# Kernel optimization log

Hardware: AMD Instinct MI355X
Metric: run time of the kernel (lower is better)

The kernel has to match this reference:

```python
import jax, jax.numpy as jnp
import numpy as np

B, N_TOKENS, E = 64, 512, 512   # batch, document tokens, embedding_dim
MAX_SEQ_LEN = 64                # decode steps


def setup_inputs() -> dict:
    key = jax.random.key(0)
    ks = jax.random.split(key, 11)
    s = 0.05
    return {
        "token_embeddings": jax.random.normal(ks[0], (B, N_TOKENS, 2 * E), jnp.float32),
        "encoded_document": jax.random.normal(ks[1], (B, 2 * E), jnp.float32),
        # LSTMCell params (hidden state is zero every step, so W_hh is dead; biases still add)
        "W_ih": jax.random.normal(ks[2], (4 * E, 2 * E), jnp.float32) * s,
        "b_ih": jax.random.normal(ks[3], (4 * E,), jnp.float32) * s,
        "b_hh": jax.random.normal(ks[4], (4 * E,), jnp.float32) * s,
        # decoder_weights: Linear(E, E)
        "Wd": jax.random.normal(ks[5], (E, E), jnp.float32) * s,
        "bd": jax.random.normal(ks[6], (E,), jnp.float32) * s,
        # encoder_weights: Linear(2E, E)
        "We": jax.random.normal(ks[7], (E, 2 * E), jnp.float32) * s,
        "be": jax.random.normal(ks[8], (E,), jnp.float32) * s,
        # reference: Linear(E, 1)
        "wr": jax.random.normal(ks[9], (1, E), jnp.float32) * s,
        "br": jax.random.normal(ks[10], (1,), jnp.float32) * s,
    }


def reference(token_embeddings, encoded_document, W_ih, b_ih, b_hh, Wd, bd, We, be, wr, br):
    b = token_embeddings.shape[0]
    batch_idx = jnp.arange(b)
    # encoder projection is loop-invariant: hoist it (same math as per-step recompute)
    enc = jnp.einsum('bnd,ed->bne', token_embeddings, We) + be  # [B, N, E]

    def lstm_zero_state(x):
        # PyTorch LSTMCell with default (zero) h, c each call
        gates = x @ W_ih.T + b_ih + b_hh  # [B, 4E]
        i, f, g, o = jnp.split(gates, 4, axis=-1)
        c = jax.nn.sigmoid(i) * jnp.tanh(g)
        return jax.nn.sigmoid(o) * jnp.tanh(c)

    def step(dec_in, _):
        hx = lstm_zero_state(dec_in)              # [B, E]
        q = hx @ Wd.T + bd                        # [B, E]
        comp = jnp.tanh(q[:, None, :] + enc)      # [B, N, E]
        scores = jnp.einsum('bne,e->bn', comp, wr[0]) + br[0]  # [B, N]
        logp = jax.nn.log_softmax(scores, axis=1)
        idx = jnp.argmax(logp, axis=1)            # [B]
        nxt = token_embeddings[batch_idx, idx]    # [B, 2E]
        return nxt, (logp, idx)

    _, (probs, idxs) = jax.lax.scan(step, encoded_document, None, length=MAX_SEQ_LEN)
    overall_probabilities = jnp.transpose(probs, (1, 0, 2))  # [B, MAX_SEQ_LEN, N]
    peak_indices = idxs.T                                     # [B, MAX_SEQ_LEN]
    return overall_probabilities, peak_indices
```

## Files before the change

kernel.cpp:

```cpp
#include <hip/hip_runtime.h>


#define DEV __device__ __forceinline__

DEV float sigm(float x) { return __fdividef(1.0f, 1.0f + __expf(-x)); }
DEV float tanh_fast(float x) {
  float e = __expf(2.0f * x);
  return 1.0f - __fdividef(2.0f, e + 1.0f);
}

#define FMA4(acc, xv, wv)                                                      \
  acc = fmaf((xv).x, (wv).x, acc); acc = fmaf((xv).y, (wv).y, acc);            \
  acc = fmaf((xv).z, (wv).z, acc); acc = fmaf((xv).w, (wv).w, acc)

__global__ __launch_bounds__(256) void kenc(const float* __restrict__ A,
                                            const float* __restrict__ Bm,
                                            const float* __restrict__ bias,
                                            float* __restrict__ C) {
  __shared__ float a_s[16][132];
  __shared__ float b_s[16][132];
  const int t = threadIdx.x;
  const int row = t >> 1;
  const int kq = (t & 1) * 8;
  const float* Arow = A + (blockIdx.x * 128 + row) * 1024 + kq;
  const float* Brow = Bm + (blockIdx.y * 128 + row) * 1024 + kq;
  const int tx = t & 15, ty = t >> 4;
  float acc[8][8] = {};
  for (int k0 = 0; k0 < 1024; k0 += 16) {
    float4 av0 = *(const float4*)(Arow + k0);
    float4 av1 = *(const float4*)(Arow + k0 + 4);
    float4 bv0 = *(const float4*)(Brow + k0);
    float4 bv1 = *(const float4*)(Brow + k0 + 4);
    __syncthreads();
    a_s[kq+0][row]=av0.x; a_s[kq+1][row]=av0.y; a_s[kq+2][row]=av0.z; a_s[kq+3][row]=av0.w;
    a_s[kq+4][row]=av1.x; a_s[kq+5][row]=av1.y; a_s[kq+6][row]=av1.z; a_s[kq+7][row]=av1.w;
    b_s[kq+0][row]=bv0.x; b_s[kq+1][row]=bv0.y; b_s[kq+2][row]=bv0.z; b_s[kq+3][row]=bv0.w;
    b_s[kq+4][row]=bv1.x; b_s[kq+5][row]=bv1.y; b_s[kq+6][row]=bv1.z; b_s[kq+7][row]=bv1.w;
    __syncthreads();
    #pragma unroll
    for (int k = 0; k < 16; ++k) {
      float a[8], b[8];
      *(float4*)(a)   = *(const float4*)&a_s[k][ty*8];
      *(float4*)(a+4) = *(const float4*)&a_s[k][ty*8+4];
      *(float4*)(b)   = *(const float4*)&b_s[k][tx*8];
      *(float4*)(b+4) = *(const float4*)&b_s[k][tx*8+4];
      #pragma unroll
      for (int i = 0; i < 8; ++i)
        #pragma unroll
        for (int j = 0; j < 8; ++j)
          acc[i][j] = fmaf(a[i], b[j], acc[i][j]);
    }
  }
  const int mb = blockIdx.x * 128 + ty * 8;
  const int eb = blockIdx.y * 128 + tx * 8;
  float bv[8];
  #pragma unroll
  for (int j = 0; j < 8; ++j) bv[j] = bias[eb + j];
  #pragma unroll
  for (int i = 0; i < 8; ++i) {
    float* orow = C + (mb + i) * 512 + eb;
    float4 o0, o1;
    o0.x=acc[i][0]+bv[0]; o0.y=acc[i][1]+bv[1]; o0.z=acc[i][2]+bv[2]; o0.w=acc[i][3]+bv[3];
    o1.x=acc[i][4]+bv[4]; o1.y=acc[i][5]+bv[5]; o1.z=acc[i][6]+bv[6]; o1.w=acc[i][7]+bv[7];
    *(float4*)orow = o0; *(float4*)(orow + 4) = o1;
  }
}

__global__ __launch_bounds__(256) void kstep_hx(
    const float* __restrict__ TE, const float* __restrict__ encd,
    const float* __restrict__ W_ih, const float* __restrict__ b_ih,
    const float* __restrict__ b_hh, const float* __restrict__ scores,
    float* __restrict__ hx, float* __restrict__ out_logp,
    float* __restrict__ out_idx, int step) {
  __shared__ int   idx_s[64];
  __shared__ float mx_s[64];
  __shared__ float wsum_s[4];
  __shared__ float part_s[4][64][6];
  const int g = blockIdx.x;
  const int t = threadIdx.x;
  const int lane = t & 63;
  const int wu = __builtin_amdgcn_readfirstlane(t >> 6);

  if (step > 0) {
    const int row = t >> 2, qq = t & 3;
    const float* srow = scores + row * 512;
    float bv = -3.0e38f; int bi = 0;
    #pragma unroll 8
    for (int n = qq; n < 512; n += 4) {
      float s = srow[n];
      if (s > bv) { bv = s; bi = n; }
    }
    #pragma unroll
    for (int m = 1; m <= 2; m <<= 1) {
      float ov = __shfl_xor(bv, m);
      int   oi = __shfl_xor(bi, m);
      if (ov > bv || (ov == bv && oi < bi)) { bv = ov; bi = oi; }
    }
    if (qq == 0) { idx_s[row] = bi; mx_s[row] = bv; }
  }
  __syncthreads();

  if (step > 0 && g < 64) {
    const float* srow = scores + g * 512;
    const float mx = mx_s[g];
    float ssum = __expf(srow[t] - mx) + __expf(srow[t + 256] - mx);
    #pragma unroll
    for (int m = 1; m <= 32; m <<= 1) ssum += __shfl_xor(ssum, m);
    if (lane == 0) wsum_s[wu] = ssum;
  }
  __syncthreads();
  if (step > 0 && g < 64) {
    const float* srow = scores + g * 512;
    const float lse = mx_s[g] + __logf(wsum_s[0] + wsum_s[1] + wsum_s[2] + wsum_s[3]);
    float* orow = out_logp + (g * 64 + (step - 1)) * 512;
    orow[t]       = srow[t]       - lse;
    orow[t + 256] = srow[t + 256] - lse;
    if (t == 0) out_idx[g * 64 + (step - 1)] = (float)idx_s[g];
  }

  const int k0 = 2 * g, k1 = 2 * g + 1;
  const int dbase = wu * 256;
  const float* p0 = W_ih + (k0        ) * 1024 + dbase;
  const float* p1 = W_ih + (k1        ) * 1024 + dbase;
  const float* p2 = W_ih + (1024 + k0) * 1024 + dbase;
  const float* p3 = W_ih + (1024 + k1) * 1024 + dbase;
  const float* p4 = W_ih + (1536 + k0) * 1024 + dbase;
  const float* p5 = W_ih + (1536 + k1) * 1024 + dbase;
  const float* xr = (step == 0) ? (encd + lane * 1024 + dbase)
                                : (TE + (lane * 512 + idx_s[lane]) * 1024 + dbase);
  float a0=0, a1=0, a2=0, a3=0, a4=0, a5=0;
  #pragma unroll 4
  for (int d = 0; d < 256; d += 4) {
    float4 xv = *(const float4*)(xr + d);
    float4 v0 = *(const float4*)(p0 + d);
    float4 v1 = *(const float4*)(p1 + d);
    float4 v2 = *(const float4*)(p2 + d);
    float4 v3 = *(const float4*)(p3 + d);
    float4 v4 = *(const float4*)(p4 + d);
    float4 v5 = *(const float4*)(p5 + d);
    FMA4(a0, xv, v0); FMA4(a1, xv, v1); FMA4(a2, xv, v2);
    FMA4(a3, xv, v3); FMA4(a4, xv, v4); FMA4(a5, xv, v5);
  }
  part_s[wu][lane][0]=a0; part_s[wu][lane][1]=a1; part_s[wu][lane][2]=a2;
  part_s[wu][lane][3]=a3; part_s[wu][lane][4]=a4; part_s[wu][lane][5]=a5;
  __syncthreads();

  if (t < 64) {
    float s0=0, s1=0, s2=0, s3=0, s4=0, s5=0;
    #pragma unroll
    for (int u = 0; u < 4; ++u) {
      s0 += part_s[u][t][0]; s1 += part_s[u][t][1]; s2 += part_s[u][t][2];
      s3 += part_s[u][t][3]; s4 += part_s[u][t][4]; s5 += part_s[u][t][5];
    }
    const float gi0 = s0 + b_ih[k0] + b_hh[k0];
    const float gi1 = s1 + b_ih[k1] + b_hh[k1];
    const float gg0 = s2 + b_ih[1024 + k0] + b_hh[1024 + k0];
    const float gg1 = s3 + b_ih[1024 + k1] + b_hh[1024 + k1];
    const float go0 = s4 + b_ih[1536 + k0] + b_hh[1536 + k0];
    const float go1 = s5 + b_ih[1536 + k1] + b_hh[1536 + k1];
    const float c0 = sigm(gi0) * tanh_fast(gg0);
    const float c1 = sigm(gi1) * tanh_fast(gg1);
    hx[t * 512 + k0] = sigm(go0) * tanh_fast(c0);
    hx[t * 512 + k1] = sigm(go1) * tanh_fast(c1);
  }
}

__global__ __launch_bounds__(256) void kq(const float* __restrict__ hx,
                                          const float* __restrict__ Wd,
                                          const float* __restrict__ bd,
                                          float* __restrict__ q) {
  __shared__ float part_s[4][64][4];
  const int g = blockIdx.x;
  const int t = threadIdx.x, lane = t & 63;
  const int wu = __builtin_amdgcn_readfirstlane(t >> 6);
  const int dbase = wu * 128;
  const int e0 = g * 4;
  const float* w0 = Wd + (e0 + 0) * 512 + dbase;
  const float* w1 = Wd + (e0 + 1) * 512 + dbase;
  const float* w2 = Wd + (e0 + 2) * 512 + dbase;
  const float* w3 = Wd + (e0 + 3) * 512 + dbase;
  const float* xr = hx + lane * 512 + dbase;
  float a0=0, a1=0, a2=0, a3=0;
  #pragma unroll 8
  for (int d = 0; d < 128; d += 4) {
    float4 xv = *(const float4*)(xr + d);
    float4 v0 = *(const float4*)(w0 + d);
    float4 v1 = *(const float4*)(w1 + d);
    float4 v2 = *(const float4*)(w2 + d);
    float4 v3 = *(const float4*)(w3 + d);
    FMA4(a0, xv, v0); FMA4(a1, xv, v1); FMA4(a2, xv, v2); FMA4(a3, xv, v3);
  }
  part_s[wu][lane][0]=a0; part_s[wu][lane][1]=a1;
  part_s[wu][lane][2]=a2; part_s[wu][lane][3]=a3;
  __syncthreads();
  if (t < 64) {
    float4 r;
    r.x = part_s[0][t][0]+part_s[1][t][0]+part_s[2][t][0]+part_s[3][t][0] + bd[e0+0];
    r.y = part_s[0][t][1]+part_s[1][t][1]+part_s[2][t][1]+part_s[3][t][1] + bd[e0+1];
    r.z = part_s[0][t][2]+part_s[1][t][2]+part_s[2][t][2]+part_s[3][t][2] + bd[e0+2];
    r.w = part_s[0][t][3]+part_s[1][t][3]+part_s[2][t][3]+part_s[3][t][3] + bd[e0+3];
    *(float4*)(q + t * 512 + e0) = r;
  }
}

__global__ __launch_bounds__(256) void kscore(const float* __restrict__ enc,
                                              const float* __restrict__ q,
                                              const float* __restrict__ wr,
                                              const float* __restrict__ br,
                                              float* __restrict__ scores) {
  const int bid = blockIdx.x;
  const int b = bid >> 3, c = bid & 7;
  const int t = threadIdx.x, lane = t & 63, w = t >> 6;
  const int le = lane & 15, nl = lane >> 4;
  float4 qv[8], wv[8];
  const float* qrow = q + b * 512 + le * 4;
  const float* wrp  = wr + le * 4;
  #pragma unroll
  for (int j = 0; j < 8; ++j) {
    qv[j] = *(const float4*)(qrow + 64 * j);
    wv[j] = *(const float4*)(wrp  + 64 * j);
  }
  const float brv = br[0];
  #pragma unroll
  for (int i = 0; i < 4; ++i) {
    const int n = c * 64 + w * 16 + i * 4 + nl;
    const float* erow = enc + (b * 512 + n) * 512 + le * 4;
    float acc = 0.0f;
    #pragma unroll
    for (int j = 0; j < 8; ++j) {
      float4 ev = *(const float4*)(erow + 64 * j);
      acc += wv[j].x * tanh_fast(qv[j].x + ev.x);
      acc += wv[j].y * tanh_fast(qv[j].y + ev.y);
      acc += wv[j].z * tanh_fast(qv[j].z + ev.z);
      acc += wv[j].w * tanh_fast(qv[j].w + ev.w);
    }
    acc += __shfl_xor(acc, 1);
    acc += __shfl_xor(acc, 2);
    acc += __shfl_xor(acc, 4);
    acc += __shfl_xor(acc, 8);
    if (le == 0) scores[b * 512 + n] = acc + brv;
  }
}

__global__ __launch_bounds__(256) void kfin(const float* __restrict__ scores,
                                            float* __restrict__ out_logp,
                                            float* __restrict__ out_idx) {
  __shared__ float mxw[4]; __shared__ int idw[4]; __shared__ float sw[4];
  const int b = blockIdx.x, t = threadIdx.x, lane = t & 63, w = t >> 6;
  const float* srow = scores + b * 512;
  const float s1 = srow[t], s2 = srow[t + 256];
  float bv; int bi;
  if (s1 >= s2) { bv = s1; bi = t; } else { bv = s2; bi = t + 256; }
  #pragma unroll
  for (int m = 1; m <= 32; m <<= 1) {
    float ov = __shfl_xor(bv, m);
    int   oi = __shfl_xor(bi, m);
    if (ov > bv || (ov == bv && oi < bi)) { bv = ov; bi = oi; }
  }
  if (lane == 0) { mxw[w] = bv; idw[w] = bi; }
  __syncthreads();
  float mx = mxw[0]; int mi = idw[0];
  #pragma unroll
  for (int u = 1; u < 4; ++u)
    if (mxw[u] > mx || (mxw[u] == mx && idw[u] < mi)) { mx = mxw[u]; mi = idw[u]; }
  float ssum = __expf(s1 - mx) + __expf(s2 - mx);
  #pragma unroll
  for (int m = 1; m <= 32; m <<= 1) ssum += __shfl_xor(ssum, m);
  if (lane == 0) sw[w] = ssum;
  __syncthreads();
  const float lse = mx + __logf(sw[0] + sw[1] + sw[2] + sw[3]);
  float* orow = out_logp + (b * 64 + 63) * 512;
  orow[t]       = s1 - lse;
  orow[t + 256] = s2 - lse;
  if (t == 0) out_idx[b * 64 + 63] = (float)mi;
}

extern "C" void kernel_launch(void* const* d_in, const int* in_sizes, int n_in,
                              void* d_out, int out_size, void* d_ws, size_t ws_size,
                              hipStream_t stream) {
  const float* TE   = (const float*)d_in[0];
  const float* encd = (const float*)d_in[1];
  const float* W_ih = (const float*)d_in[2];
  const float* b_ih = (const float*)d_in[3];
  const float* b_hh = (const float*)d_in[4];
  const float* Wd   = (const float*)d_in[5];
  const float* bd   = (const float*)d_in[6];
  const float* We   = (const float*)d_in[7];
  const float* be   = (const float*)d_in[8];
  const float* wr   = (const float*)d_in[9];
  const float* br   = (const float*)d_in[10];

  float* out     = (float*)d_out;
  float* out_idx = out + 64 * 64 * 512;

  float* enc    = (float*)d_ws;
  float* scores = enc + 16777216;
  float* hx     = scores + 32768;
  float* q      = hx + 32768;

  kenc<<<dim3(256, 4), 256, 0, stream>>>(TE, We, be, enc);
  for (int t = 0; t < 64; ++t) {
    kstep_hx<<<256, 256, 0, stream>>>(TE, encd, W_ih, b_ih, b_hh, scores, hx,
                                      out, out_idx, t);
    kq<<<128, 256, 0, stream>>>(hx, Wd, bd, q);
    kscore<<<512, 256, 0, stream>>>(enc, q, wr, br, scores);
  }
  kfin<<<64, 256, 0, stream>>>(scores, out, out_idx);
}
```

Before: 3.762 ms.

## Fuse decode loop into one persistent cooperative kernel with grid barriers

```diff
diff --git a/kernel.cpp b/kernel.cpp
--- a/kernel.cpp
+++ b/kernel.cpp
@@ -40,10 +40,10 @@
     #pragma unroll
     for (int k = 0; k < 16; ++k) {
       float a[8], b[8];
-      *(float4*)(a)   = *(const float4*)&a_s[k][ty*8];
-      *(float4*)(a+4) = *(const float4*)&a_s[k][ty*8+4];
-      *(float4*)(b)   = *(const float4*)&b_s[k][tx*8];
-      *(float4*)(b+4) = *(const float4*)&b_s[k][tx*8+4];
+      *(float4*)(a)   = *(const float4*)&a_s[k][ty*4];
+      *(float4*)(a+4) = *(const float4*)&a_s[k][64 + ty*4];
+      *(float4*)(b)   = *(const float4*)&b_s[k][tx*4];
+      *(float4*)(b+4) = *(const float4*)&b_s[k][64 + tx*4];
       #pragma unroll
       for (int i = 0; i < 8; ++i)
         #pragma unroll
@@ -51,228 +51,212 @@
           acc[i][j] = fmaf(a[i], b[j], acc[i][j]);
     }
   }
-  const int mb = blockIdx.x * 128 + ty * 8;
-  const int eb = blockIdx.y * 128 + tx * 8;
-  float bv[8];
-  #pragma unroll
-  for (int j = 0; j < 8; ++j) bv[j] = bias[eb + j];
+  const int mb = blockIdx.x * 128;
+  const int eb = blockIdx.y * 128;
+  float4 bv0 = *(const float4*)&bias[eb + tx*4];
+  float4 bv1 = *(const float4*)&bias[eb + 64 + tx*4];
   #pragma unroll
   for (int i = 0; i < 8; ++i) {
-    float* orow = C + (mb + i) * 512 + eb;
+    const int r = mb + ((i < 4) ? (ty*4 + i) : (64 + ty*4 + (i - 4)));
+    float* orow = C + r * 512 + eb;
     float4 o0, o1;
-    o0.x=acc[i][0]+bv[0]; o0.y=acc[i][1]+bv[1]; o0.z=acc[i][2]+bv[2]; o0.w=acc[i][3]+bv[3];
-    o1.x=acc[i][4]+bv[4]; o1.y=acc[i][5]+bv[5]; o1.z=acc[i][6]+bv[6]; o1.w=acc[i][7]+bv[7];
-    *(float4*)orow = o0; *(float4*)(orow + 4) = o1;
-  }
-}
-
-__global__ __launch_bounds__(256) void kstep_hx(
+    o0.x=acc[i][0]+bv0.x; o0.y=acc[i][1]+bv0.y; o0.z=acc[i][2]+bv0.z; o0.w=acc[i][3]+bv0.w;
+    o1.x=acc[i][4]+bv1.x; o1.y=acc[i][5]+bv1.y; o1.z=acc[i][6]+bv1.z; o1.w=acc[i][7]+bv1.w;
+    *(float4*)(orow + tx*4) = o0;
+    *(float4*)(orow + 64 + tx*4) = o1;
+  }
+}
+
+DEV void gbar(unsigned* bar) {
+  __syncthreads();
+  if (threadIdx.x == 0) {
+    unsigned g0 = __hip_atomic_load(bar + 16, __ATOMIC_RELAXED, __HIP_MEMORY_SCOPE_AGENT);
+    __threadfence();
+    unsigned a = __hip_atomic_fetch_add(bar, 1u, __ATOMIC_ACQ_REL, __HIP_MEMORY_SCOPE_AGENT);
+    if (a == 255u) {
+      __hip_atomic_store(bar, 0u, __ATOMIC_RELAXED, __HIP_MEMORY_SCOPE_AGENT);
+      __hip_atomic_fetch_add(bar + 16, 1u, __ATOMIC_RELEASE, __HIP_MEMORY_SCOPE_AGENT);
+    } else {
+      while (__hip_atomic_load(bar + 16, __ATOMIC_ACQUIRE, __HIP_MEMORY_SCOPE_AGENT) == g0)
+        __builtin_amdgcn_s_sleep(2);
+    }
+    __threadfence();
+  }
+  __syncthreads();
+}
+
+__global__ __launch_bounds__(256) void kloop(
     const float* __restrict__ TE, const float* __restrict__ encd,
     const float* __restrict__ W_ih, const float* __restrict__ b_ih,
-    const float* __restrict__ b_hh, const float* __restrict__ scores,
-    float* __restrict__ hx, float* __restrict__ out_logp,
-    float* __restrict__ out_idx, int step) {
+    const float* __restrict__ b_hh, const float* __restrict__ Wd,
+    const float* __restrict__ bd, const float* __restrict__ wr,
+    const float* __restrict__ br, const float* __restrict__ enc,
+    float* __restrict__ scores, float* __restrict__ hx, float* __restrict__ q,
+    unsigned* __restrict__ bar, float* __restrict__ out_logp,
+    float* __restrict__ out_idx) {
   __shared__ int   idx_s[64];
   __shared__ float mx_s[64];
   __shared__ float wsum_s[4];
   __shared__ float part_s[4][64][6];
+  __shared__ float partq_s[4][64][4];
   const int g = blockIdx.x;
   const int t = threadIdx.x;
   const int lane = t & 63;
   const int wu = __builtin_amdgcn_readfirstlane(t >> 6);
 
-  if (step > 0) {
-    const int row = t >> 2, qq = t & 3;
-    const float* srow = scores + row * 512;
-    float bv = -3.0e38f; int bi = 0;
-    #pragma unroll 8
-    for (int n = qq; n < 512; n += 4) {
-      float s = srow[n];
-      if (s > bv) { bv = s; bi = n; }
-    }
-    #pragma unroll
-    for (int m = 1; m <= 2; m <<= 1) {
-      float ov = __shfl_xor(bv, m);
-      int   oi = __shfl_xor(bi, m);
-      if (ov > bv || (ov == bv && oi < bi)) { bv = ov; bi = oi; }
-    }
-    if (qq == 0) { idx_s[row] = bi; mx_s[row] = bv; }
-  }
-  __syncthreads();
-
-  if (step > 0 && g < 64) {
-    const float* srow = scores + g * 512;
-    const float mx = mx_s[g];
-    float ssum = __expf(srow[t] - mx) + __expf(srow[t + 256] - mx);
-    #pragma unroll
-    for (int m = 1; m <= 32; m <<= 1) ssum += __shfl_xor(ssum, m);
-    if (lane == 0) wsum_s[wu] = ssum;
-  }
-  __syncthreads();
-  if (step > 0 && g < 64) {
-    const float* srow = scores + g * 512;
-    const float lse = mx_s[g] + __logf(wsum_s[0] + wsum_s[1] + wsum_s[2] + wsum_s[3]);
-    float* orow = out_logp + (g * 64 + (step - 1)) * 512;
-    orow[t]       = srow[t]       - lse;
-    orow[t + 256] = srow[t + 256] - lse;
-    if (t == 0) out_idx[g * 64 + (step - 1)] = (float)idx_s[g];
-  }
-
-  const int k0 = 2 * g, k1 = 2 * g + 1;
-  const int dbase = wu * 256;
-  const float* p0 = W_ih + (k0        ) * 1024 + dbase;
-  const float* p1 = W_ih + (k1        ) * 1024 + dbase;
-  const float* p2 = W_ih + (1024 + k0) * 1024 + dbase;
-  const float* p3 = W_ih + (1024 + k1) * 1024 + dbase;
-  const float* p4 = W_ih + (1536 + k0) * 1024 + dbase;
-  const float* p5 = W_ih + (1536 + k1) * 1024 + dbase;
-  const float* xr = (step == 0) ? (encd + lane * 1024 + dbase)
-                                : (TE + (lane * 512 + idx_s[lane]) * 1024 + dbase);
-  float a0=0, a1=0, a2=0, a3=0, a4=0, a5=0;
-  #pragma unroll 4
-  for (int d = 0; d < 256; d += 4) {
-    float4 xv = *(const float4*)(xr + d);
-    float4 v0 = *(const float4*)(p0 + d);
-    float4 v1 = *(const float4*)(p1 + d);
-    float4 v2 = *(const float4*)(p2 + d);
-    float4 v3 = *(const float4*)(p3 + d);
-    float4 v4 = *(const float4*)(p4 + d);
-    float4 v5 = *(const float4*)(p5 + d);
-    FMA4(a0, xv, v0); FMA4(a1, xv, v1); FMA4(a2, xv, v2);
-    FMA4(a3, xv, v3); FMA4(a4, xv, v4); FMA4(a5, xv, v5);
-  }
-  part_s[wu][lane][0]=a0; part_s[wu][lane][1]=a1; part_s[wu][lane][2]=a2;
-  part_s[wu][lane][3]=a3; part_s[wu][lane][4]=a4; part_s[wu][lane][5]=a5;
-  __syncthreads();
-
-  if (t < 64) {
-    float s0=0, s1=0, s2=0, s3=0, s4=0, s5=0;
-    #pragma unroll
-    for (int u = 0; u < 4; ++u) {
-      s0 += part_s[u][t][0]; s1 += part_s[u][t][1]; s2 += part_s[u][t][2];
-      s3 += part_s[u][t][3]; s4 += part_s[u][t][4]; s5 += part_s[u][t][5];
-    }
-    const float gi0 = s0 + b_ih[k0] + b_hh[k0];
-    const float gi1 = s1 + b_ih[k1] + b_hh[k1];
-    const float gg0 = s2 + b_ih[1024 + k0] + b_hh[1024 + k0];
-    const float gg1 = s3 + b_ih[1024 + k1] + b_hh[1024 + k1];
-    const float go0 = s4 + b_ih[1536 + k0] + b_hh[1536 + k0];
-    const float go1 = s5 + b_ih[1536 + k1] + b_hh[1536 + k1];
-    const float c0 = sigm(gi0) * tanh_fast(gg0);
-    const float c1 = sigm(gi1) * tanh_fast(gg1);
-    hx[t * 512 + k0] = sigm(go0) * tanh_fast(c0);
-    hx[t * 512 + k1] = sigm(go1) * tanh_fast(c1);
-  }
-}
-
-__global__ __launch_bounds__(256) void kq(const float* __restrict__ hx,
-                                          const float* __restrict__ Wd,
-                                          const float* __restrict__ bd,
-                                          float* __restrict__ q) {
-  __shared__ float part_s[4][64][4];
-  const int g = blockIdx.x;
-  const int t = threadIdx.x, lane = t & 63;
-  const int wu = __builtin_amdgcn_readfirstlane(t >> 6);
-  const int dbase = wu * 128;
-  const int e0 = g * 4;
-  const float* w0 = Wd + (e0 + 0) * 512 + dbase;
-  const float* w1 = Wd + (e0 + 1) * 512 + dbase;
-  const float* w2 = Wd + (e0 + 2) * 512 + dbase;
-  const float* w3 = Wd + (e0 + 3) * 512 + dbase;
-  const float* xr = hx + lane * 512 + dbase;
-  float a0=0, a1=0, a2=0, a3=0;
-  #pragma unroll 8
-  for (int d = 0; d < 128; d += 4) {
-    float4 xv = *(const float4*)(xr + d);
-    float4 v0 = *(const float4*)(w0 + d);
-    float4 v1 = *(const float4*)(w1 + d);
-    float4 v2 = *(const float4*)(w2 + d);
-    float4 v3 = *(const float4*)(w3 + d);
-    FMA4(a0, xv, v0); FMA4(a1, xv, v1); FMA4(a2, xv, v2); FMA4(a3, xv, v3);
-  }
-  part_s[wu][lane][0]=a0; part_s[wu][lane][1]=a1;
-  part_s[wu][lane][2]=a2; part_s[wu][lane][3]=a3;
-  __syncthreads();
-  if (t < 64) {
-    float4 r;
-    r.x = part_s[0][t][0]+part_s[1][t][0]+part_s[2][t][0]+part_s[3][t][0] + bd[e0+0];
-    r.y = part_s[0][t][1]+part_s[1][t][1]+part_s[2][t][1]+part_s[3][t][1] + bd[e0+1];
-    r.z = part_s[0][t][2]+part_s[1][t][2]+part_s[2][t][2]+part_s[3][t][2] + bd[e0+2];
-    r.w = part_s[0][t][3]+part_s[1][t][3]+part_s[2][t][3]+part_s[3][t][3] + bd[e0+3];
-    *(float4*)(q + t * 512 + e0) = r;
-  }
-}
-
-__global__ __launch_bounds__(256) void kscore(const float* __restrict__ enc,
-                                              const float* __restrict__ q,
-                                              const float* __restrict__ wr,
-                                              const float* __restrict__ br,
-                                              float* __restrict__ scores) {
-  const int bid = blockIdx.x;
-  const int b = bid >> 3, c = bid & 7;
-  const int t = threadIdx.x, lane = t & 63, w = t >> 6;
+  const int sb = g >> 2, sc = g & 3;
   const int le = lane & 15, nl = lane >> 4;
-  float4 qv[8], wv[8];
-  const float* qrow = q + b * 512 + le * 4;
-  const float* wrp  = wr + le * 4;
+  float4 wv[8];
   #pragma unroll
-  for (int j = 0; j < 8; ++j) {
-    qv[j] = *(const float4*)(qrow + 64 * j);
-    wv[j] = *(const float4*)(wrp  + 64 * j);
-  }
+  for (int j = 0; j < 8; ++j) wv[j] = *(const float4*)(wr + le * 4 + 64 * j);
   const float brv = br[0];
-  #pragma unroll
-  for (int i = 0; i < 4; ++i) {
-    const int n = c * 64 + w * 16 + i * 4 + nl;
-    const float* erow = enc + (b * 512 + n) * 512 + le * 4;
-    float acc = 0.0f;
-    #pragma unroll
-    for (int j = 0; j < 8; ++j) {
-      float4 ev = *(const float4*)(erow + 64 * j);
-      acc += wv[j].x * tanh_fast(qv[j].x + ev.x);
-      acc += wv[j].y * tanh_fast(qv[j].y + ev.y);
-      acc += wv[j].z * tanh_fast(qv[j].z + ev.z);
-      acc += wv[j].w * tanh_fast(qv[j].w + ev.w);
-    }
-    acc += __shfl_xor(acc, 1);
-    acc += __shfl_xor(acc, 2);
-    acc += __shfl_xor(acc, 4);
-    acc += __shfl_xor(acc, 8);
-    if (le == 0) scores[b * 512 + n] = acc + brv;
-  }
-}
-
-__global__ __launch_bounds__(256) void kfin(const float* __restrict__ scores,
-                                            float* __restrict__ out_logp,
-                                            float* __restrict__ out_idx) {
-  __shared__ float mxw[4]; __shared__ int idw[4]; __shared__ float sw[4];
-  const int b = blockIdx.x, t = threadIdx.x, lane = t & 63, w = t >> 6;
-  const float* srow = scores + b * 512;
-  const float s1 = srow[t], s2 = srow[t + 256];
-  float bv; int bi;
-  if (s1 >= s2) { bv = s1; bi = t; } else { bv = s2; bi = t + 256; }
-  #pragma unroll
-  for (int m = 1; m <= 32; m <<= 1) {
-    float ov = __shfl_xor(bv, m);
-    int   oi = __shfl_xor(bi, m);
-    if (ov > bv || (ov == bv && oi < bi)) { bv = ov; bi = oi; }
-  }
-  if (lane == 0) { mxw[w] = bv; idw[w] = bi; }
-  __syncthreads();
-  float mx = mxw[0]; int mi = idw[0];
-  #pragma unroll
-  for (int u = 1; u < 4; ++u)
-    if (mxw[u] > mx || (mxw[u] == mx && idw[u] < mi)) { mx = mxw[u]; mi = idw[u]; }
-  float ssum = __expf(s1 - mx) + __expf(s2 - mx);
-  #pragma unroll
-  for (int m = 1; m <= 32; m <<= 1) ssum += __shfl_xor(ssum, m);
-  if (lane == 0) sw[w] = ssum;
-  __syncthreads();
-  const float lse = mx + __logf(sw[0] + sw[1] + sw[2] + sw[3]);
-  float* orow = out_logp + (b * 64 + 63) * 512;
-  orow[t]       = s1 - lse;
-  orow[t + 256] = s2 - lse;
-  if (t == 0) out_idx[b * 64 + 63] = (float)mi;
+
+  for (int step = 0; step <= 64; ++step) {
+    if (step > 0) {
+      const int row = t >> 2, qq = t & 3;
+      const float* srow = scores + row * 512;
+      float bv = -3.0e38f; int bi = 0;
+      #pragma unroll 8
+      for (int n = qq; n < 512; n += 4) {
+        float s = srow[n];
+        if (s > bv) { bv = s; bi = n; }
+      }
+      #pragma unroll
+      for (int m = 1; m <= 2; m <<= 1) {
+        float ov = __shfl_xor(bv, m);
+        int   oi = __shfl_xor(bi, m);
+        if (ov > bv || (ov == bv && oi < bi)) { bv = ov; bi = oi; }
+      }
+      if (qq == 0) { idx_s[row] = bi; mx_s[row] = bv; }
+    }
+    __syncthreads();
+
+    if (step > 0 && g < 64) {
+      const float* srow = scores + g * 512;
+      const float mx = mx_s[g];
+      float ssum = __expf(srow[t] - mx) + __expf(srow[t + 256] - mx);
+      #pragma unroll
+      for (int m = 1; m <= 32; m <<= 1) ssum += __shfl_xor(ssum, m);
+      if (lane == 0) wsum_s[wu] = ssum;
+    }
+    __syncthreads();
+    if (step > 0 && g < 64) {
+      const float* srow = scores + g * 512;
+      const float lse = mx_s[g] + __logf(wsum_s[0] + wsum_s[1] + wsum_s[2] + wsum_s[3]);
+      float* orow = out_logp + (g * 64 + (step - 1)) * 512;
+      orow[t]       = srow[t]       - lse;
+      orow[t + 256] = srow[t + 256] - lse;
+      if (t == 0) out_idx[g * 64 + (step - 1)] = (float)idx_s[g];
+    }
+    if (step == 64) break;
+
+    {
+      const int k0 = 2 * g, k1 = 2 * g + 1;
+      const int dbase = wu * 256;
+      const float* p0 = W_ih + (k0        ) * 1024 + dbase;
+      const float* p1 = W_ih + (k1        ) * 1024 + dbase;
+      const float* p2 = W_ih + (1024 + k0) * 1024 + dbase;
+      const float* p3 = W_ih + (1024 + k1) * 1024 + dbase;
+      const float* p4 = W_ih + (1536 + k0) * 1024 + dbase;
+      const float* p5 = W_ih + (1536 + k1) * 1024 + dbase;
+      const float* xr = (step == 0) ? (encd + lane * 1024 + dbase)
+                                    : (TE + (lane * 512 + idx_s[lane]) * 1024 + dbase);
+      float a0=0, a1=0, a2=0, a3=0, a4=0, a5=0;
+      #pragma unroll 4
+      for (int d = 0; d < 256; d += 4) {
+        float4 xv = *(const float4*)(xr + d);
+        float4 v0 = *(const float4*)(p0 + d);
+        float4 v1 = *(const float4*)(p1 + d);
+        float4 v2 = *(const float4*)(p2 + d);
+        float4 v3 = *(const float4*)(p3 + d);
+        float4 v4 = *(const float4*)(p4 + d);
+        float4 v5 = *(const float4*)(p5 + d);
+        FMA4(a0, xv, v0); FMA4(a1, xv, v1); FMA4(a2, xv, v2);
+        FMA4(a3, xv, v3); FMA4(a4, xv, v4); FMA4(a5, xv, v5);
+      }
+      part_s[wu][lane][0]=a0; part_s[wu][lane][1]=a1; part_s[wu][lane][2]=a2;
+      part_s[wu][lane][3]=a3; part_s[wu][lane][4]=a4; part_s[wu][lane][5]=a5;
+      __syncthreads();
+      if (t < 64) {
+        float s0=0, s1=0, s2=0, s3=0, s4=0, s5=0;
+        #pragma unroll
+        for (int u = 0; u < 4; ++u) {
+          s0 += part_s[u][t][0]; s1 += part_s[u][t][1]; s2 += part_s[u][t][2];
+          s3 += part_s[u][t][3]; s4 += part_s[u][t][4]; s5 += part_s[u][t][5];
+        }
+        const float gi0 = s0 + b_ih[k0] + b_hh[k0];
+        const float gi1 = s1 + b_ih[k1] + b_hh[k1];
+        const float gg0 = s2 + b_ih[1024 + k0] + b_hh[1024 + k0];
+        const float gg1 = s3 + b_ih[1024 + k1] + b_hh[1024 + k1];
+        const float go0 = s4 + b_ih[1536 + k0] + b_hh[1536 + k0];
+        const float go1 = s5 + b_ih[1536 + k1] + b_hh[1536 + k1];
+        const float c0 = sigm(gi0) * tanh_fast(gg0);
+        const float c1 = sigm(gi1) * tanh_fast(gg1);
+        hx[t * 512 + k0] = sigm(go0) * tanh_fast(c0);
+        hx[t * 512 + k1] = sigm(go1) * tanh_fast(c1);
+      }
+    }
+    gbar(bar);
+
+    if (g < 128) {
+      const int dbase = wu * 128;
+      const int e0 = g * 4;
+      const float* w0 = Wd + (e0 + 0) * 512 + dbase;
+      const float* w1 = Wd + (e0 + 1) * 512 + dbase;
+      const float* w2 = Wd + (e0 + 2) * 512 + dbase;
+      const float* w3 = Wd + (e0 + 3) * 512 + dbase;
+      const float* xr = hx + lane * 512 + dbase;
+      float a0=0, a1=0, a2=0, a3=0;
+      #pragma unroll 8
+      for (int d = 0; d < 128; d += 4) {
+        float4 xv = *(const float4*)(xr + d);
+        float4 v0 = *(const float4*)(w0 + d);
+        float4 v1 = *(const float4*)(w1 + d);
+        float4 v2 = *(const float4*)(w2 + d);
+        float4 v3 = *(const float4*)(w3 + d);
+        FMA4(a0, xv, v0); FMA4(a1, xv, v1); FMA4(a2, xv, v2); FMA4(a3, xv, v3);
+      }
+      partq_s[wu][lane][0]=a0; partq_s[wu][lane][1]=a1;
+      partq_s[wu][lane][2]=a2; partq_s[wu][lane][3]=a3;
+      __syncthreads();
+      if (t < 64) {
+        float4 r;
+        r.x = partq_s[0][t][0]+partq_s[1][t][0]+partq_s[2][t][0]+partq_s[3][t][0] + bd[e0+0];
+        r.y = partq_s[0][t][1]+partq_s[1][t][1]+partq_s[2][t][1]+partq_s[3][t][1] + bd[e0+1];
+        r.z = partq_s[0][t][2]+partq_s[1][t][2]+partq_s[2][t][2]+partq_s[3][t][2] + bd[e0+2];
+        r.w = partq_s[0][t][3]+partq_s[1][t][3]+partq_s[2][t][3]+partq_s[3][t][3] + bd[e0+3];
+        *(float4*)(q + t * 512 + e0) = r;
+      }
+    }
+    gbar(bar);
+
+    {
+      float4 qv[8];
+      const float* qrow = q + sb * 512 + le * 4;
+      #pragma unroll
+      for (int j = 0; j < 8; ++j) qv[j] = *(const float4*)(qrow + 64 * j);
+      #pragma unroll
+      for (int i = 0; i < 8; ++i) {
+        const int n = sc * 128 + wu * 32 + i * 4 + nl;
+        const float* erow = enc + (sb * 512 + n) * 512 + le * 4;
+        float acc = 0.0f;
+        #pragma unroll
+        for (int j = 0; j < 8; ++j) {
+          float4 ev = *(const float4*)(erow + 64 * j);
+          acc += wv[j].x * tanh_fast(qv[j].x + ev.x);
+          acc += wv[j].y * tanh_fast(qv[j].y + ev.y);
+          acc += wv[j].z * tanh_fast(qv[j].z + ev.z);
+          acc += wv[j].w * tanh_fast(qv[j].w + ev.w);
+        }
+        acc += __shfl_xor(acc, 1);
+        acc += __shfl_xor(acc, 2);
+        acc += __shfl_xor(acc, 4);
+        acc += __shfl_xor(acc, 8);
+        if (le == 0) scores[sb * 512 + n] = acc + brv;
+      }
+    }
+    gbar(bar);
+  }
 }
 
 extern "C" void kernel_launch(void* const* d_in, const int* in_sizes, int n_in,
@@ -293,17 +277,18 @@
   float* out     = (float*)d_out;
   float* out_idx = out + 64 * 64 * 512;
 
-  float* enc    = (float*)d_ws;
-  float* scores = enc + 16777216;
-  float* hx     = scores + 32768;
-  float* q      = hx + 32768;
-
+  float* enc     = (float*)d_ws;
+  float* scores  = enc + 16777216;
+  float* hx      = scores + 32768;
+  float* q       = hx + 32768;
+  unsigned* bar  = (unsigned*)(q + 32768);
+
+  hipMemsetAsync(bar, 0, 256, stream);
   kenc<<<dim3(256, 4), 256, 0, stream>>>(TE, We, be, enc);
-  for (int t = 0; t < 64; ++t) {
-    kstep_hx<<<256, 256, 0, stream>>>(TE, encd, W_ih, b_ih, b_hh, scores, hx,
-                                      out, out_idx, t);
-    kq<<<128, 256, 0, stream>>>(hx, Wd, bd, q);
-    kscore<<<512, 256, 0, stream>>>(enc, q, wr, br, scores);
-  }
-  kfin<<<64, 256, 0, stream>>>(scores, out, out_idx);
-}
+
+  void* args[] = {(void*)&TE, (void*)&encd, (void*)&W_ih, (void*)&b_ih,
+                  (void*)&b_hh, (void*)&Wd, (void*)&bd, (void*)&wr,
+                  (void*)&br, (void*)&enc, (void*)&scores, (void*)&hx,
+                  (void*)&q, (void*)&bar, (void*)&out, (void*)&out_idx};
+  hipLaunchCooperativeKernel((void*)kloop, dim3(256), dim3(256), args, 0, stream);
+}
```

Result: slower. 10.66 ms (+183.3%).
